# Kernel optimization log

Hardware: AMD Instinct MI355X
Metric: run time of the kernel (lower is better)

## Reference

```python
import jax, jax.numpy as jnp
import numpy as np

SEQ, BATCH = 64, 32
X_DIM, Z_DIM, Y_DIM, H_DIM, N_LAYERS = 32, 128, 16, 128, 3
PARAM_SHAPES = [(H_DIM, X_DIM), (H_DIM,), (H_DIM, H_DIM), (H_DIM,), (Y_DIM, H_DIM), (Y_DIM,)]
SIZES = [int(np.prod(s)) for s in PARAM_SHAPES]
NBLOCKS = [(s + Z_DIM - 1) // Z_DIM for s in SIZES]
OFFSETS = np.cumsum([0] + NBLOCKS)          # static block offsets per param tensor
TOTAL_NB = int(OFFSETS[-1])                  # 179 fastfood blocks total


def fwht(x):
    """Unnormalized Walsh-Hadamard transform over last axis (power-of-2 dim)."""
    d = x.shape[-1]
    h = 2
    while h <= d:
        x = x.reshape(x.shape[:-1] + (d // h, h))
        a, b = x[..., : h // 2], x[..., h // 2:]
        x = jnp.concatenate([a + b, a - b], axis=-1).reshape(x.shape[:-2] + (d,))
        h *= 2
    return x


def setup_inputs() -> dict:
    key = jax.random.key(0)
    ks = jax.random.split(key, 16)
    inp = {
        "x": jax.random.normal(ks[0], (SEQ, BATCH, X_DIM), jnp.float32),
        "z": jax.random.normal(ks[1], (SEQ, BATCH, Z_DIM), jnp.float32),
    }
    # base MLP parameters (nn.Linear default init: U(-1/sqrt(fan_in), 1/sqrt(fan_in)))
    for i in range(N_LAYERS):
        w_shape, b_shape = PARAM_SHAPES[2 * i], PARAM_SHAPES[2 * i + 1]
        s = 1.0 / np.sqrt(w_shape[1])
        inp[f"W0_{i}"] = jax.random.uniform(ks[2 + 2 * i], w_shape, jnp.float32, -s, s)
        inp[f"b0_{i}"] = jax.random.uniform(ks[3 + 2 * i], b_shape, jnp.float32, -s, s)
    # FastFood params stacked over all blocks of all param tensors
    inp["ffB"] = jnp.where(jax.random.bernoulli(ks[10], 0.5, (TOTAL_NB, Z_DIM)), 1.0, -1.0).astype(jnp.float32)
    inp["ffG"] = jax.random.normal(ks[11], (TOTAL_NB, Z_DIM), jnp.float32)
    inp["ffS"] = jax.random.normal(ks[12], (TOTAL_NB, Z_DIM), jnp.float32) * 0.01
    inp["ffP"] = jnp.argsort(jax.random.uniform(ks[13], (TOTAL_NB, Z_DIM)), axis=-1).astype(jnp.int32)
    return inp


def reference(x, z, W0_0, b0_0, W0_1, b0_1, W0_2, b0_2, ffB, ffG, ffS, ffP):
    N = SEQ * BATCH
    zf = z.reshape(N, Z_DIM)
    # FastFood upsample for all blocks at once: S * H * G * Pi * H * B * z
    v = ffB[None] * zf[:, None, :]                       # (N, NB, d)
    v = fwht(v)
    rows = jnp.arange(TOTAL_NB)[:, None]
    v = v[:, rows, ffP]                                  # per-block permutation
    v = ffG[None] * v
    v = fwht(v)
    v = ffS[None] * v / Z_DIM                            # (N, NB, d)

    Ws, bs = [W0_0, W0_1, W0_2], [b0_0, b0_1, b0_2]
    h = x
    for i in range(N_LAYERS):
        wi, bi = 2 * i, 2 * i + 1
        wd = v[:, OFFSETS[wi]:OFFSETS[wi + 1], :].reshape(N, -1)[:, :SIZES[wi]]
        wd = wd.reshape(SEQ, BATCH, *PARAM_SHAPES[wi])
        bd = v[:, OFFSETS[bi]:OFFSETS[bi + 1], :].reshape(N, -1)[:, :SIZES[bi]]
        bd = bd.reshape(SEQ, BATCH, *PARAM_SHAPES[bi])
        w = Ws[i][None, None] + wd                       # (seq, batch, out, in)
        b = bs[i][None, None] + bd                       # (seq, batch, out)
        h = jnp.einsum('sbi,sbji->sbj', h, w) + b
        if i < N_LAYERS - 1:
            h = jax.nn.relu(h)
    return h
```

## Files before the change

### kernel.cpp

```cpp
#include <hip/hip_runtime.h>
#include <hip/hip_fp16.h>


#define NTOK 2048
#define SLOT (128 * 2048)

typedef _Float16 f16x8 __attribute__((ext_vector_type(8)));
typedef float f32x4 __attribute__((ext_vector_type(4)));
typedef unsigned int u32;

__device__ __forceinline__ float2 pk_add(float2 a, float2 b) {
  float2 d;
  asm("v_pk_add_f32 %0, %1, %2" : "=v"(d) : "v"(a), "v"(b));
  return d;
}
__device__ __forceinline__ float2 pk_sub(float2 a, float2 b) {
  float2 d;
  asm("v_pk_add_f32 %0, %1, %2 neg_lo:[0,1] neg_hi:[0,1]" : "=v"(d) : "v"(a), "v"(b));
  return d;
}

__device__ __forceinline__ void fwht128p(float2 w[64]) {
#pragma unroll
  for (int m = 0; m < 64; m++) {
    float a = w[m].x, b = w[m].y;
    w[m].x = a + b; w[m].y = a - b;
  }
#pragma unroll
  for (int sig = 1; sig < 64; sig <<= 1) {
#pragma unroll
    for (int m = 0; m < 64; m++) {
      if ((m & sig) == 0) {
        float2 a = w[m], b = w[m + sig];
        w[m] = pk_add(a, b);
        w[m + sig] = pk_sub(a, b);
      }
    }
  }
}

__global__ __launch_bounds__(64) void kx(const float* __restrict__ x,
                                         float* __restrict__ xT) {
  const int t = blockIdx.x * 64 + threadIdx.x;
  const float4* x4 = (const float4*)(x + (size_t)t * 32);
#pragma unroll
  for (int k = 0; k < 8; k++) {
    float4 f = x4[k];
    xT[(size_t)(4 * k + 0) * NTOK + t] = f.x;
    xT[(size_t)(4 * k + 1) * NTOK + t] = f.y;
    xT[(size_t)(4 * k + 2) * NTOK + t] = f.z;
    xT[(size_t)(4 * k + 3) * NTOK + t] = f.w;
  }
}

__global__ __launch_bounds__(128) void km(
    const float* __restrict__ ffB, const float* __restrict__ ffG,
    const float* __restrict__ ffS, const int* __restrict__ ffP,
    _Float16* __restrict__ M) {
  __shared__ _Float16 T[128 * 128];
  __shared__ float sG[128], sS[128];
  __shared__ int sP[128];
  const int tid = threadIdx.x;
  const int j = blockIdx.x;
  sG[tid] = ffG[(size_t)j * 128 + tid];
  sS[tid] = ffS[(size_t)j * 128 + tid];
  sP[tid] = ffP[(size_t)j * 128 + tid];
  __syncthreads();
  const float Bc = ffB[(size_t)j * 128 + tid];
  float2 w[64];
#pragma unroll
  for (int m = 0; m < 64; m++) {
    int p0 = sP[2 * m], p1 = sP[2 * m + 1];
    float s0 = (__popc(p0 & tid) & 1) ? -Bc : Bc;
    float s1 = (__popc(p1 & tid) & 1) ? -Bc : Bc;
    w[m].x = sG[2 * m] * s0;
    w[m].y = sG[2 * m + 1] * s1;
  }
  fwht128p(w);
#pragma unroll
  for (int m = 0; m < 64; m++) {
    T[(2 * m) * 128 + tid] = (_Float16)(w[m].x * sS[2 * m] * 0.0078125f);
    T[(2 * m + 1) * 128 + tid] = (_Float16)(w[m].y * sS[2 * m + 1] * 0.0078125f);
  }
  __syncthreads();
  const u32* Ts = (const u32*)T;
  u32* Mo = (u32*)(M + (size_t)j * 16384);
#pragma unroll 4
  for (int i = 0; i < 64; i++) Mo[i * 128 + tid] = Ts[i * 128 + tid];
}

template <int MODE, int JB>
__global__ __launch_bounds__(256, 2) void gf(
    const _Float16* __restrict__ M, const float* __restrict__ z,
    int j0, int js,
    const float* __restrict__ aux0,
    const float* __restrict__ aux1,
    const float* __restrict__ aux2,
    const _Float16* __restrict__ auxY,
    float* __restrict__ outp,
    _Float16* __restrict__ yout) {
  __shared__ _Float16 Asm[128 * 136];
  __shared__ _Float16 Bsm[128 * 136];
  const int tid = threadIdx.x;
  const int lane = tid & 63, wv = tid >> 6;
  const int ln = lane & 15, g = lane >> 4;
  const int strip = blockIdx.x;

  {
    const float4* zg = (const float4*)z + (size_t)(strip * 128) * 32;
#pragma unroll
    for (int i = 0; i < 16; i++) {
      int F = i * 256 + tid;
      int t = F >> 5, q = F & 31;
      float4 f = zg[(size_t)t * 32 + q];
      __half2 hlo = __floats2half2_rn(f.x, f.y);
      __half2 hhi = __floats2half2_rn(f.z, f.w);
      uint2 u = make_uint2(*(u32*)&hlo, *(u32*)&hhi);
      *(uint2*)(&Bsm[t * 136 + q * 4]) = u;
    }
  }

#pragma unroll 1
  for (int jj = 0; jj < JB; jj++) {
    const int j = j0 + (blockIdx.y * JB + jj) * js;
    {
      const uint4* Mg = (const uint4*)(M + (size_t)j * 16384);
#pragma unroll
      for (int i = 0; i < 8; i++) {
        int F = i * 256 + tid;
        int v = F >> 4, c = F & 15;
        uint4 q4 = Mg[F];
        *(uint4*)(&Asm[v * 136 + c * 8]) = q4;
      }
    }
    __syncthreads();

    f32x4 acc[8][2];
#pragma unroll
    for (int vt = 0; vt < 8; vt++)
#pragma unroll
      for (int tt = 0; tt < 2; tt++) {
        f32x4 zf = {0.f, 0.f, 0.f, 0.f};
        acc[vt][tt] = zf;
      }

#pragma unroll
    for (int ks = 0; ks < 4; ks++) {
      f16x8 af[8], bf[2];
#pragma unroll
      for (int vt = 0; vt < 8; vt++)
        af[vt] = *(const f16x8*)(&Asm[(vt * 16 + ln) * 136 + ks * 32 + g * 8]);
#pragma unroll
      for (int tt = 0; tt < 2; tt++)
        bf[tt] = *(const f16x8*)(&Bsm[(wv * 32 + tt * 16 + ln) * 136 + ks * 32 + g * 8]);
#pragma unroll
      for (int vt = 0; vt < 8; vt++)
#pragma unroll
        for (int tt = 0; tt < 2; tt++)
          acc[vt][tt] = __builtin_amdgcn_mfma_f32_16x16x32_f16(af[vt], bf[tt],
                                                               acc[vt][tt], 0, 0, 0);
    }

    const int tg0 = strip * 128 + wv * 32 + ln;

    if constexpr (MODE == 3) {
      _Float16* yd = yout + (size_t)blockIdx.y * SLOT;
#pragma unroll
      for (int vt = 0; vt < 8; vt++)
#pragma unroll
        for (int tt = 0; tt < 2; tt++)
#pragma unroll
          for (int r = 0; r < 4; r++)
            yd[(size_t)(vt * 16 + g * 4 + r) * NTOK + tg0 + tt * 16] =
                (_Float16)acc[vt][tt][r];
    } else if constexpr (MODE == 0) {
      float pw[2][4] = {{0, 0, 0, 0}, {0, 0, 0, 0}};
      float pb[2][4] = {{0, 0, 0, 0}, {0, 0, 0, 0}};
#pragma unroll
      for (int vt = 0; vt < 8; vt++) {
        const int rho = vt >> 1;
#pragma unroll
        for (int r = 0; r < 4; r++) {
          int i = (vt & 1) * 16 + g * 4 + r;
          float w0v = aux1[(4 * j + rho) * 32 + i];
          float x0 = aux0[(size_t)i * NTOK + tg0];
          float x1 = aux0[(size_t)i * NTOK + tg0 + 16];
          pw[0][rho] += acc[vt][0][r] * x0; pb[0][rho] += w0v * x0;
          pw[1][rho] += acc[vt][1][r] * x1; pb[1][rho] += w0v * x1;
        }
      }
#pragma unroll
      for (int tt = 0; tt < 2; tt++)
#pragma unroll
        for (int rho = 0; rho < 4; rho++) {
          pw[tt][rho] += __shfl_xor(pw[tt][rho], 16);
          pw[tt][rho] += __shfl_xor(pw[tt][rho], 32);
          pb[tt][rho] += __shfl_xor(pb[tt][rho], 16);
          pb[tt][rho] += __shfl_xor(pb[tt][rho], 32);
        }
      if (g == 0) {
#pragma unroll
        for (int tt = 0; tt < 2; tt++)
#pragma unroll
          for (int rho = 0; rho < 4; rho++) {
            int rr = 4 * j + rho, tgs = tg0 + tt * 16;
            float bd = (float)auxY[(size_t)rr * NTOK + tgs];
            float val = pb[tt][rho] + pw[tt][rho] + aux2[rr] + bd;
            outp[(size_t)rr * NTOK + tgs] = fmaxf(val, 0.f);
          }
      }
    } else {
      const int row = (MODE == 1) ? (j - 33) : (j - 162);
      float pw0 = 0.f, pw1 = 0.f, pb0 = 0.f, pb1 = 0.f;
#pragma unroll
      for (int vt = 0; vt < 8; vt++)
#pragma unroll
        for (int r = 0; r < 4; r++) {
          int v = vt * 16 + g * 4 + r;
          float wv_ = aux1[row * 128 + v];
          float h0 = aux0[(size_t)v * NTOK + tg0];
          float h1v = aux0[(size_t)v * NTOK + tg0 + 16];
          pw0 += acc[vt][0][r] * h0; pb0 += wv_ * h0;
          pw1 += acc[vt][1][r] * h1v; pb1 += wv_ * h1v;
        }
      pw0 += __shfl_xor(pw0, 16); pw0 += __shfl_xor(pw0, 32);
      pw1 += __shfl_xor(pw1, 16); pw1 += __shfl_xor(pw1, 32);
      pb0 += __shfl_xor(pb0, 16); pb0 += __shfl_xor(pb0, 32);
      pb1 += __shfl_xor(pb1, 16); pb1 += __shfl_xor(pb1, 32);
      if (g == 0) {
        float bias = aux2[row];
        float bd0 = (float)auxY[(size_t)row * NTOK + tg0];
        float bd1 = (float)auxY[(size_t)row * NTOK + tg0 + 16];
        float v0 = pb0 + pw0 + bias + bd0;
        float v1 = pb1 + pw1 + bias + bd1;
        if constexpr (MODE == 1) {
          outp[(size_t)row * NTOK + tg0] = fmaxf(v0, 0.f);
          outp[(size_t)row * NTOK + tg0 + 16] = fmaxf(v1, 0.f);
        } else {
          outp[(size_t)tg0 * 16 + row] = v0;
          outp[(size_t)(tg0 + 16) * 16 + row] = v1;
        }
      }
    }
    __syncthreads();
  }
}

extern "C" void kernel_launch(void* const* d_in, const int* in_sizes, int n_in,
                              void* d_out, int out_size, void* d_ws, size_t ws_size,
                              hipStream_t stream) {
  const float* x  = (const float*)d_in[0];
  const float* z  = (const float*)d_in[1];
  const float* W0 = (const float*)d_in[2];
  const float* b0 = (const float*)d_in[3];
  const float* W1 = (const float*)d_in[4];
  const float* b1 = (const float*)d_in[5];
  const float* W2 = (const float*)d_in[6];
  const float* b2 = (const float*)d_in[7];
  const float* fB = (const float*)d_in[8];
  const float* fG = (const float*)d_in[9];
  const float* fS = (const float*)d_in[10];
  const int*   fP = (const int*)d_in[11];
  float* out = (float*)d_out;
  (void)ws_size;

  char* p = (char*)d_ws;
  _Float16* Mbuf  = (_Float16*)p; p += (size_t)179 * 16384 * 2;
  _Float16* Ybias = (_Float16*)p; p += (size_t)3 * SLOT * 2;
  float* xT = (float*)p;          p += (size_t)32 * NTOK * 4;
  float* h1 = (float*)p;          p += (size_t)128 * NTOK * 4;
  float* h2 = (float*)p;          p += (size_t)128 * NTOK * 4;

  kx<<<dim3(32), 64, 0, stream>>>(x, xT);
  km<<<dim3(179), 128, 0, stream>>>(fB, fG, fS, fP, Mbuf);
  gf<3, 1><<<dim3(16, 2), 256, 0, stream>>>(Mbuf, z, 32, 129,
      nullptr, nullptr, nullptr, nullptr, nullptr, Ybias);
  gf<3, 1><<<dim3(16, 1), 256, 0, stream>>>(Mbuf, z, 178, 0,
      nullptr, nullptr, nullptr, nullptr, nullptr, Ybias + 2 * SLOT);
  gf<0, 2><<<dim3(16, 16), 256, 0, stream>>>(Mbuf, z, 0, 1,
      xT, W0, b0, Ybias, h1, nullptr);
  gf<1, 2><<<dim3(16, 64), 256, 0, stream>>>(Mbuf, z, 33, 1,
      h1, W1, b1, Ybias + SLOT, h2, nullptr);
  gf<2, 2><<<dim3(16, 8), 256, 0, stream>>>(Mbuf, z, 162, 1,
      h2, W2, b2, Ybias + 2 * SLOT, out, nullptr);
}
```

Measured before the change: 126.2 us.

## Fuse fastfood bias rows into layer kernels and switch activations to token-major

The separate kernels that precomputed the fastfood bias deltas (Ybias) and the x transpose kernel are removed. Each layer kernel now computes its bias delta inline as a small dot product between a staged M bias row and the z tile already in shared memory. Activations h1/h2 are stored token-major so they can be read as float4 vectors, and weights are staged in shared memory. This cuts three launches and the Ybias write/read traffic, at the cost of extra scalar FMAs per block and uncoalesced scalar stores in layer 1.

```diff
diff --git a/kernel.cpp b/kernel.cpp
--- a/kernel.cpp
+++ b/kernel.cpp
@@ -3,9 +3,9 @@
 
 
 #define NTOK 2048
-#define SLOT (128 * 2048)
 
 typedef _Float16 f16x8 __attribute__((ext_vector_type(8)));
+typedef _Float16 f16x4 __attribute__((ext_vector_type(4)));
 typedef float f32x4 __attribute__((ext_vector_type(4)));
 typedef unsigned int u32;
 
@@ -36,20 +36,6 @@
         w[m + sig] = pk_sub(a, b);
       }
     }
-  }
-}
-
-__global__ __launch_bounds__(64) void kx(const float* __restrict__ x,
-                                         float* __restrict__ xT) {
-  const int t = blockIdx.x * 64 + threadIdx.x;
-  const float4* x4 = (const float4*)(x + (size_t)t * 32);
-#pragma unroll
-  for (int k = 0; k < 8; k++) {
-    float4 f = x4[k];
-    xT[(size_t)(4 * k + 0) * NTOK + t] = f.x;
-    xT[(size_t)(4 * k + 1) * NTOK + t] = f.y;
-    xT[(size_t)(4 * k + 2) * NTOK + t] = f.z;
-    xT[(size_t)(4 * k + 3) * NTOK + t] = f.w;
   }
 }
 
@@ -92,19 +78,21 @@
 template <int MODE, int JB>
 __global__ __launch_bounds__(256, 2) void gf(
     const _Float16* __restrict__ M, const float* __restrict__ z,
-    int j0, int js,
-    const float* __restrict__ aux0,
-    const float* __restrict__ aux1,
-    const float* __restrict__ aux2,
-    const _Float16* __restrict__ auxY,
-    float* __restrict__ outp,
-    _Float16* __restrict__ yout) {
+    int j0, int jbias,
+    const float* __restrict__ xin,
+    const float* __restrict__ hin,
+    const float* __restrict__ Wp, const float* __restrict__ bp,
+    float* __restrict__ outp) {
   __shared__ _Float16 Asm[128 * 136];
   __shared__ _Float16 Bsm[128 * 136];
+  __shared__ _Float16 pM[4 * 136];
+  __shared__ float pW[128];
   const int tid = threadIdx.x;
   const int lane = tid & 63, wv = tid >> 6;
   const int ln = lane & 15, g = lane >> 4;
   const int strip = blockIdx.x;
+  const int tl0 = wv * 32 + ln;
+  const int tg0 = strip * 128 + tl0;
 
   {
     const float4* zg = (const float4*)z + (size_t)(strip * 128) * 32;
@@ -120,18 +108,43 @@
     }
   }
 
+  float4 xa[2][2];
+  if constexpr (MODE == 0) {
+#pragma unroll
+    for (int tt = 0; tt < 2; tt++) {
+      const float* xr = xin + (size_t)(tg0 + tt * 16) * 32;
+      xa[tt][0] = *(const float4*)(xr + g * 4);
+      xa[tt][1] = *(const float4*)(xr + 16 + g * 4);
+    }
+  }
+
 #pragma unroll 1
   for (int jj = 0; jj < JB; jj++) {
-    const int j = j0 + (blockIdx.y * JB + jj) * js;
+    const int row = blockIdx.y * JB + jj;
+    const int j = j0 + row;
+
     {
       const uint4* Mg = (const uint4*)(M + (size_t)j * 16384);
 #pragma unroll
       for (int i = 0; i < 8; i++) {
         int F = i * 256 + tid;
         int v = F >> 4, c = F & 15;
-        uint4 q4 = Mg[F];
-        *(uint4*)(&Asm[v * 136 + c * 8]) = q4;
-      }
+        *(uint4*)(&Asm[v * 136 + c * 8]) = Mg[F];
+      }
+    }
+    if constexpr (MODE == 0) {
+      {
+        const u32* src = (const u32*)(M + (size_t)jbias * 16384 + (size_t)(4 * j) * 128);
+        int rr = tid >> 6, uu = tid & 63;
+        *(u32*)(&pM[rr * 136 + uu * 2]) = src[rr * 64 + uu];
+      }
+      if (tid < 128) pW[tid] = Wp[(size_t)(4 * j) * 32 + tid];
+    } else {
+      if (tid < 64) {
+        const u32* src = (const u32*)(M + (size_t)jbias * 16384 + (size_t)row * 128);
+        *(u32*)(&pM[tid * 2]) = src[tid];
+      }
+      if (tid < 128) pW[tid] = Wp[(size_t)row * 128 + tid];
     }
     __syncthreads();
 
@@ -143,7 +156,6 @@
         f32x4 zf = {0.f, 0.f, 0.f, 0.f};
         acc[vt][tt] = zf;
       }
-
 #pragma unroll
     for (int ks = 0; ks < 4; ks++) {
       f16x8 af[8], bf[2];
@@ -161,32 +173,37 @@
                                                                acc[vt][tt], 0, 0, 0);
     }
 
-    const int tg0 = strip * 128 + wv * 32 + ln;
-
-    if constexpr (MODE == 3) {
-      _Float16* yd = yout + (size_t)blockIdx.y * SLOT;
-#pragma unroll
-      for (int vt = 0; vt < 8; vt++)
-#pragma unroll
-        for (int tt = 0; tt < 2; tt++)
-#pragma unroll
-          for (int r = 0; r < 4; r++)
-            yd[(size_t)(vt * 16 + g * 4 + r) * NTOK + tg0 + tt * 16] =
-                (_Float16)acc[vt][tt][r];
-    } else if constexpr (MODE == 0) {
+    if constexpr (MODE == 0) {
       float pw[2][4] = {{0, 0, 0, 0}, {0, 0, 0, 0}};
       float pb[2][4] = {{0, 0, 0, 0}, {0, 0, 0, 0}};
 #pragma unroll
       for (int vt = 0; vt < 8; vt++) {
         const int rho = vt >> 1;
+        const float4 w4 = *(const float4*)&pW[rho * 32 + (vt & 1) * 16 + g * 4];
 #pragma unroll
         for (int r = 0; r < 4; r++) {
-          int i = (vt & 1) * 16 + g * 4 + r;
-          float w0v = aux1[(4 * j + rho) * 32 + i];
-          float x0 = aux0[(size_t)i * NTOK + tg0];
-          float x1 = aux0[(size_t)i * NTOK + tg0 + 16];
-          pw[0][rho] += acc[vt][0][r] * x0; pb[0][rho] += w0v * x0;
-          pw[1][rho] += acc[vt][1][r] * x1; pb[1][rho] += w0v * x1;
+          const float* xp0 = &xa[0][vt & 1].x;
+          const float* xp1 = &xa[1][vt & 1].x;
+          const float* wp4 = &w4.x;
+          pw[0][rho] += acc[vt][0][r] * xp0[r];
+          pw[1][rho] += acc[vt][1][r] * xp1[r];
+          pb[0][rho] += wp4[r] * xp0[r];
+          pb[1][rho] += wp4[r] * xp1[r];
+        }
+      }
+#pragma unroll
+      for (int tt = 0; tt < 2; tt++) {
+#pragma unroll
+        for (int uu = 0; uu < 8; uu++) {
+          int u0 = g * 32 + uu * 4;
+          f16x4 zh = *(const f16x4*)(&Bsm[(tl0 + tt * 16) * 136 + u0]);
+          float zf0 = (float)zh[0], zf1 = (float)zh[1], zf2 = (float)zh[2], zf3 = (float)zh[3];
+#pragma unroll
+          for (int rho = 0; rho < 4; rho++) {
+            f16x4 mh = *(const f16x4*)(&pM[rho * 136 + u0]);
+            pw[tt][rho] += (float)mh[0] * zf0 + (float)mh[1] * zf1 +
+                           (float)mh[2] * zf2 + (float)mh[3] * zf3;
+          }
         }
       }
 #pragma unroll
@@ -200,42 +217,57 @@
         }
       if (g == 0) {
 #pragma unroll
-        for (int tt = 0; tt < 2; tt++)
-#pragma unroll
-          for (int rho = 0; rho < 4; rho++) {
-            int rr = 4 * j + rho, tgs = tg0 + tt * 16;
-            float bd = (float)auxY[(size_t)rr * NTOK + tgs];
-            float val = pb[tt][rho] + pw[tt][rho] + aux2[rr] + bd;
-            outp[(size_t)rr * NTOK + tgs] = fmaxf(val, 0.f);
-          }
+        for (int tt = 0; tt < 2; tt++) {
+          float4 o;
+          float* op = &o.x;
+#pragma unroll
+          for (int rho = 0; rho < 4; rho++)
+            op[rho] = fmaxf(pb[tt][rho] + pw[tt][rho] + bp[4 * j + rho], 0.f);
+          *(float4*)(outp + (size_t)(tg0 + tt * 16) * 128 + 4 * j) = o;
+        }
       }
     } else {
-      const int row = (MODE == 1) ? (j - 33) : (j - 162);
       float pw0 = 0.f, pw1 = 0.f, pb0 = 0.f, pb1 = 0.f;
 #pragma unroll
-      for (int vt = 0; vt < 8; vt++)
+      for (int vt = 0; vt < 8; vt++) {
+        const int v0 = vt * 16 + g * 4;
+        const float4 w4 = *(const float4*)&pW[v0];
+        const float4 h0 = *(const float4*)(hin + (size_t)tg0 * 128 + v0);
+        const float4 h1v = *(const float4*)(hin + (size_t)(tg0 + 16) * 128 + v0);
+        const float* wp4 = &w4.x;
+        const float* hp0 = &h0.x;
+        const float* hp1 = &h1v.x;
 #pragma unroll
         for (int r = 0; r < 4; r++) {
-          int v = vt * 16 + g * 4 + r;
-          float wv_ = aux1[row * 128 + v];
-          float h0 = aux0[(size_t)v * NTOK + tg0];
-          float h1v = aux0[(size_t)v * NTOK + tg0 + 16];
-          pw0 += acc[vt][0][r] * h0; pb0 += wv_ * h0;
-          pw1 += acc[vt][1][r] * h1v; pb1 += wv_ * h1v;
-        }
+          pw0 += acc[vt][0][r] * hp0[r];
+          pw1 += acc[vt][1][r] * hp1[r];
+          pb0 += wp4[r] * hp0[r];
+          pb1 += wp4[r] * hp1[r];
+        }
+      }
+#pragma unroll
+      for (int uu = 0; uu < 8; uu++) {
+        int u0 = g * 32 + uu * 4;
+        f16x4 mh = *(const f16x4*)(&pM[u0]);
+        f16x4 z0 = *(const f16x4*)(&Bsm[tl0 * 136 + u0]);
+        f16x4 z1 = *(const f16x4*)(&Bsm[(tl0 + 16) * 136 + u0]);
+#pragma unroll
+        for (int e = 0; e < 4; e++) {
+          pw0 += (float)mh[e] * (float)z0[e];
+          pw1 += (float)mh[e] * (float)z1[e];
+        }
+      }
       pw0 += __shfl_xor(pw0, 16); pw0 += __shfl_xor(pw0, 32);
       pw1 += __shfl_xor(pw1, 16); pw1 += __shfl_xor(pw1, 32);
       pb0 += __shfl_xor(pb0, 16); pb0 += __shfl_xor(pb0, 32);
       pb1 += __shfl_xor(pb1, 16); pb1 += __shfl_xor(pb1, 32);
       if (g == 0) {
-        float bias = aux2[row];
-        float bd0 = (float)auxY[(size_t)row * NTOK + tg0];
-        float bd1 = (float)auxY[(size_t)row * NTOK + tg0 + 16];
-        float v0 = pb0 + pw0 + bias + bd0;
-        float v1 = pb1 + pw1 + bias + bd1;
+        float bias = bp[row];
+        float v0 = pb0 + pw0 + bias;
+        float v1 = pb1 + pw1 + bias;
         if constexpr (MODE == 1) {
-          outp[(size_t)row * NTOK + tg0] = fmaxf(v0, 0.f);
-          outp[(size_t)row * NTOK + tg0 + 16] = fmaxf(v1, 0.f);
+          outp[(size_t)tg0 * 128 + row] = fmaxf(v0, 0.f);
+          outp[(size_t)(tg0 + 16) * 128 + row] = fmaxf(v1, 0.f);
         } else {
           outp[(size_t)tg0 * 16 + row] = v0;
           outp[(size_t)(tg0 + 16) * 16 + row] = v1;
@@ -265,22 +297,12 @@
   (void)ws_size;
 
   char* p = (char*)d_ws;
-  _Float16* Mbuf  = (_Float16*)p; p += (size_t)179 * 16384 * 2;
-  _Float16* Ybias = (_Float16*)p; p += (size_t)3 * SLOT * 2;
-  float* xT = (float*)p;          p += (size_t)32 * NTOK * 4;
-  float* h1 = (float*)p;          p += (size_t)128 * NTOK * 4;
-  float* h2 = (float*)p;          p += (size_t)128 * NTOK * 4;
-
-  kx<<<dim3(32), 64, 0, stream>>>(x, xT);
+  _Float16* Mbuf = (_Float16*)p; p += (size_t)179 * 16384 * 2;
+  float* h1 = (float*)p;         p += (size_t)NTOK * 128 * 4;
+  float* h2 = (float*)p;         p += (size_t)NTOK * 128 * 4;
+
   km<<<dim3(179), 128, 0, stream>>>(fB, fG, fS, fP, Mbuf);
-  gf<3, 1><<<dim3(16, 2), 256, 0, stream>>>(Mbuf, z, 32, 129,
-      nullptr, nullptr, nullptr, nullptr, nullptr, Ybias);
-  gf<3, 1><<<dim3(16, 1), 256, 0, stream>>>(Mbuf, z, 178, 0,
-      nullptr, nullptr, nullptr, nullptr, nullptr, Ybias + 2 * SLOT);
-  gf<0, 2><<<dim3(16, 16), 256, 0, stream>>>(Mbuf, z, 0, 1,
-      xT, W0, b0, Ybias, h1, nullptr);
-  gf<1, 2><<<dim3(16, 64), 256, 0, stream>>>(Mbuf, z, 33, 1,
-      h1, W1, b1, Ybias + SLOT, h2, nullptr);
-  gf<2, 2><<<dim3(16, 8), 256, 0, stream>>>(Mbuf, z, 162, 1,
-      h2, W2, b2, Ybias + 2 * SLOT, out, nullptr);
-}
+  gf<0, 2><<<dim3(16, 16), 256, 0, stream>>>(Mbuf, z, 0, 32, x, nullptr, W0, b0, h1);
+  gf<1, 2><<<dim3(16, 64), 256, 0, stream>>>(Mbuf, z, 33, 161, nullptr, h1, W1, b1, h2);
+  gf<2, 2><<<dim3(16, 8), 256, 0, stream>>>(Mbuf, z, 162, 178, nullptr, h2, W2, b2, out);
+}
```

After: 126.1 us. About the same (-0.0%).
